# Kernel optimization log

Measured on AMD Instinct MI355X. Metric: run time of the kernel, lower is better.

## Reference

```python
import jax, jax.numpy as jnp
import numpy as np

B, S, W, H = 16, 512, 8, 768  # batch, seq_len, max_span width, hidden_dim


def setup_inputs() -> dict:
    key = jax.random.key(0)
    ks = jax.random.split(key, 6)
    return {
        "hidden": jax.random.normal(ks[0], (B, S, H), jnp.float32),
        "term_weight": jax.random.normal(ks[1], (H,), jnp.float32),
        "w1": jax.random.normal(ks[2], (H, 64), jnp.float32) * 0.02,
        "b1": jnp.zeros((64,), jnp.float32),
        "w2": jax.random.normal(ks[3], (64, 1), jnp.float32) * 0.05,
        "b2": jnp.zeros((1,), jnp.float32),
        "w_score": jax.random.normal(ks[4], (H, 2), jnp.float32) * 0.02,
        "b_score": jnp.zeros((2,), jnp.float32),
    }


def reference(hidden, term_weight, w1, b1, w2, b2, w_score, b_score):
    # TermAttention token logits: MLP(hidden * termWeight) depends only on the
    # token, not the span, so compute once per token instead of per span.
    ah = hidden * term_weight                                  # [B,S,H]
    tok_logit = (jax.nn.relu(ah @ w1 + b1) @ w2 + b2)[..., 0]  # [B,S]

    starts = jnp.arange(S)
    offs = jnp.arange(W)
    # candidate span (start s, width w) covers tokens s .. min(s+w, S-1)
    tok_idx = jnp.minimum(starts[:, None] + offs[None, :], S - 1)      # [S,W]
    span_len = jnp.minimum(offs[None, :] + 1, S - starts[:, None])    # [S,W]

    Lg = tok_logit[:, tok_idx]   # [B,S,W] gathered per-position logits
    Hg = hidden[:, tok_idx]      # [B,S,W,H] gathered per-position hiddens

    # pos_mask[s,w,j] = position j is inside span (s, width w)
    pos_mask = offs[None, None, :] < span_len[:, :, None]              # [S,W,W]
    logits = jnp.where(pos_mask[None], Lg[:, :, None, :], -jnp.inf)   # [B,S,W,W]
    attn = jax.nn.softmax(logits, axis=-1)                             # [B,S,W,W]

    # span embedding = attention-weighted sum of span token hiddens
    emb = jnp.einsum('bswj,bsjh->bswh', attn, Hg)                      # [B,S,W,H]
    scores = emb @ w_score + b_score                                   # [B,S,W,2]
    return scores
```

## Files before the change

kernel.cpp:

```cpp
#include <hip/hip_runtime.h>

#define S_LEN 512
#define H_DIM 768
#define BS_TOK 8192
#define NCOLS 80
#define KSPLIT 4
#define KSEG 192
#define KPAD 200
#define PSTRIDE 72
#define BM 32
#define TOKB 32

typedef __attribute__((ext_vector_type(8))) short short8v;
typedef __attribute__((ext_vector_type(4))) short short4v;
typedef __attribute__((ext_vector_type(4))) float f32x4;
typedef __attribute__((ext_vector_type(4))) _Float16 h4;

__device__ __forceinline__ short f2bf(float f) {
  union { float f; unsigned u; } x; x.f = f;
  unsigned r = x.u + 0x7fffu + ((x.u >> 16) & 1u);
  return (short)(r >> 16);
}

__global__ __launch_bounds__(128) void k1f(const float* __restrict__ hidden,
                                           const float* __restrict__ tw,
                                           const float* __restrict__ w1,
                                           const float* __restrict__ wsc,
                                           _Float16* __restrict__ part) {
  __shared__ short bs[NCOLS * KPAD];
  const int tid  = threadIdx.x;
  const int bid  = blockIdx.x;
  const int tile = bid >> 2;
  const int kseg = bid & 3;
  const int k0   = kseg * KSEG;

#pragma unroll
  for (int i = 0; i < 24; ++i) {
    int e = tid + 128 * i;
    int koff = e >> 4, c4 = e & 15;
    int k = k0 + koff;
    float twk = tw[k];
    float4 w = *reinterpret_cast<const float4*>(w1 + (size_t)k * 64 + c4 * 4);
    bs[(c4 * 4 + 0) * KPAD + koff] = f2bf(w.x * twk);
    bs[(c4 * 4 + 1) * KPAD + koff] = f2bf(w.y * twk);
    bs[(c4 * 4 + 2) * KPAD + koff] = f2bf(w.z * twk);
    bs[(c4 * 4 + 3) * KPAD + koff] = f2bf(w.w * twk);
  }
#pragma unroll
  for (int i = 0; i < 3; ++i) {
    int e = tid + 128 * i;
    if (e < 2 * KSEG) {
      int koff = e >> 1, c = e & 1;
      bs[(64 + c) * KPAD + koff] = f2bf(wsc[(size_t)(k0 + koff) * 2 + c]);
    }
  }
  for (int i = tid; i < 14 * KSEG; i += 128) {
    int c = 66 + i / KSEG, koff = i - (c - 66) * KSEG;
    bs[c * KPAD + koff] = 0;
  }
  __syncthreads();

  const int w    = tid >> 6;
  const int lane = tid & 63;
  const int ci   = lane & 15;
  const int g    = lane >> 4;
  const int kg   = g * 8;
  const int r0   = tile * BM + w * 16;

  f32x4 acc[5];
#pragma unroll
  for (int nt = 0; nt < 5; ++nt) acc[nt] = (f32x4){0.f, 0.f, 0.f, 0.f};

  const float* aptr = hidden + (size_t)(r0 + ci) * H_DIM + k0 + kg;
#pragma unroll
  for (int ks = 0; ks < KSEG; ks += 32) {
    float4 a0 = *reinterpret_cast<const float4*>(aptr + ks);
    float4 a1 = *reinterpret_cast<const float4*>(aptr + ks + 4);
    short8v av;
    av[0] = f2bf(a0.x); av[1] = f2bf(a0.y); av[2] = f2bf(a0.z); av[3] = f2bf(a0.w);
    av[4] = f2bf(a1.x); av[5] = f2bf(a1.y); av[6] = f2bf(a1.z); av[7] = f2bf(a1.w);
#pragma unroll
    for (int nt = 0; nt < 5; ++nt) {
      short8v bb = *reinterpret_cast<const short8v*>(&bs[(nt * 16 + ci) * KPAD + ks + kg]);
      acc[nt] = __builtin_amdgcn_mfma_f32_16x16x32_bf16(av, bb, acc[nt], 0, 0, 0);
    }
  }

  _Float16* pr = part + ((size_t)kseg * BS_TOK + r0) * PSTRIDE;
#pragma unroll
  for (int j = 0; j < 4; ++j) {
    int r = 4 * g + j;
#pragma unroll
    for (int nt = 0; nt < 4; ++nt)
      pr[r * PSTRIDE + nt * 16 + ci] = (_Float16)acc[nt][j];
    if (ci < 2) pr[r * PSTRIDE + 64 + ci] = (_Float16)acc[4][j];
  }
}

__global__ __launch_bounds__(256) void kB(const _Float16* __restrict__ part,
                                          const float* __restrict__ b1,
                                          const float* __restrict__ w2,
                                          const float* __restrict__ b2,
                                          const float* __restrict__ bsc,
                                          float* __restrict__ out) {
  __shared__ float lp[TOKB + 8][4];
  const int tid  = threadIdx.x;
  const int t0   = blockIdx.x * TOKB;
  const int w    = tid >> 6;
  const int lane = tid & 63;
  const int ci   = lane & 15;
  const int grp  = lane >> 4;
  const int base = w * 4 + grp;

#pragma unroll
  for (int pass = 0; pass < 3; ++pass) {
    int slot = pass * 16 + base;
    if (slot < TOKB + 7) {
      int tt = min(t0 + slot, BS_TOK - 1);
      f32x4 s = (f32x4){0.f, 0.f, 0.f, 0.f};
#pragma unroll
      for (int seg = 0; seg < KSPLIT; ++seg) {
        h4 v = *reinterpret_cast<const h4*>(
            part + ((size_t)seg * BS_TOK + tt) * PSTRIDE + 4 * ci);
        s[0] += (float)v[0]; s[1] += (float)v[1];
        s[2] += (float)v[2]; s[3] += (float)v[3];
      }
      const float4 bb = *reinterpret_cast<const float4*>(b1 + 4 * ci);
      const float4 ww = *reinterpret_cast<const float4*>(w2 + 4 * ci);
      float r = fmaxf(s[0] + bb.x, 0.f) * ww.x + fmaxf(s[1] + bb.y, 0.f) * ww.y +
                fmaxf(s[2] + bb.z, 0.f) * ww.z + fmaxf(s[3] + bb.w, 0.f) * ww.w;
#pragma unroll
      for (int msk = 1; msk < 16; msk <<= 1) r += __shfl_xor(r, msk, 64);
      if (ci == 0) lp[slot][0] = r + b2[0];
      if (ci < 2) {
        float pv = 0.f;
#pragma unroll
        for (int seg = 0; seg < KSPLIT; ++seg)
          pv += (float)part[((size_t)seg * BS_TOK + tt) * PSTRIDE + 64 + ci];
        lp[slot][1 + ci] = pv;
      }
    }
  }
  __syncthreads();

  if (tid < TOKB) {
    int t = t0 + tid;
    int s_ = t & (S_LEN - 1);
    int nmax = min(8, S_LEN - s_);
    float bs0 = bsc[0], bs1 = bsc[1];
    float m = lp[tid][0];
    float d = 1.f;
    float n0 = lp[tid][1], n1 = lp[tid][2];
    float o[16];
    o[0] = n0 + bs0; o[1] = n1 + bs1;
#pragma unroll
    for (int j = 1; j < 8; ++j) {
      if (j < nmax) {
        float L  = lp[tid + j][0];
        float nm = fmaxf(m, L);
        float sc = __expf(m - nm);
        float e  = __expf(L - nm);
        d  = d  * sc + e;
        n0 = n0 * sc + e * lp[tid + j][1];
        n1 = n1 * sc + e * lp[tid + j][2];
        m = nm;
      }
      float inv = 1.f / d;
      o[2 * j]     = n0 * inv + bs0;
      o[2 * j + 1] = n1 * inv + bs1;
    }
    float4* op = reinterpret_cast<float4*>(out + (size_t)t * 16);
#pragma unroll
    for (int i = 0; i < 4; ++i) op[i] = *reinterpret_cast<float4*>(&o[4 * i]);
  }
}


__global__ __launch_bounds__(256) void kprep(const float* __restrict__ tw,
                                             const float* __restrict__ w1,
                                             const float* __restrict__ wsc,
                                             short* __restrict__ wcat) {
  int i = blockIdx.x * 256 + threadIdx.x;
  if (i >= NCOLS * H_DIM) return;
  int c = i / H_DIM, k = i - c * H_DIM;
  float v = 0.f;
  if (c < 64)       v = tw[k] * w1[k * 64 + c];
  else if (c == 64) v = wsc[k * 2 + 0];
  else if (c == 65) v = wsc[k * 2 + 1];
  wcat[i] = f2bf(v);
}

__global__ __launch_bounds__(256) void k1s(const float* __restrict__ hidden,
                                           const short* __restrict__ wcat,
                                           const float* __restrict__ b1,
                                           const float* __restrict__ w2,
                                           const float* __restrict__ b2,
                                           float* __restrict__ logit,
                                           float* __restrict__ pbuf) {
  __shared__ short as[64 * 72];
  __shared__ short bss[NCOLS * 72];
  const int tid  = threadIdx.x;
  const int t0   = blockIdx.x * 64;
  const int w    = tid >> 6;
  const int lane = tid & 63;
  const int ci   = lane & 15;
  const int kg   = (lane >> 4) * 8;
  const int arow = w * 16 + ci;

  f32x4 acc[5];
#pragma unroll
  for (int nt = 0; nt < 5; ++nt) acc[nt] = (f32x4){0.f, 0.f, 0.f, 0.f};

  for (int cc = 0; cc < H_DIM / 64; ++cc) {
    const int k0 = cc * 64;
    __syncthreads();
#pragma unroll
    for (int i = 0; i < 4; ++i) {
      int f = tid + 256 * i;
      int r = f >> 4, c4 = f & 15;
      const float4 v = *reinterpret_cast<const float4*>(
          hidden + (size_t)(t0 + r) * H_DIM + k0 + c4 * 4);
      short4v bv;
      bv[0] = f2bf(v.x); bv[1] = f2bf(v.y); bv[2] = f2bf(v.z); bv[3] = f2bf(v.w);
      *reinterpret_cast<short4v*>(&as[r * 72 + c4 * 4]) = bv;
    }
    for (int i = tid; i < NCOLS * 8; i += 256) {
      int r = i >> 3, c8 = i & 7;
      short8v v = *reinterpret_cast<const short8v*>(wcat + r * H_DIM + k0 + c8 * 8);
      *reinterpret_cast<short8v*>(&bss[r * 72 + c8 * 8]) = v;
    }
    __syncthreads();
#pragma unroll
    for (int ks = 0; ks < 64; ks += 32) {
      short8v a = *reinterpret_cast<const short8v*>(&as[arow * 72 + ks + kg]);
#pragma unroll
      for (int nt = 0; nt < 5; ++nt) {
        short8v bb = *reinterpret_cast<const short8v*>(&bss[(nt * 16 + ci) * 72 + ks + kg]);
        acc[nt] = __builtin_amdgcn_mfma_f32_16x16x32_bf16(a, bb, acc[nt], 0, 0, 0);
      }
    }
  }

  const int g = lane >> 4;
  float lg[4];
#pragma unroll
  for (int j = 0; j < 4; ++j) {
    float sacc = 0.f;
#pragma unroll
    for (int nt = 0; nt < 4; ++nt) {
      int c = nt * 16 + ci;
      float z = acc[nt][j] + b1[c];
      z = fmaxf(z, 0.f);
      sacc += z * w2[c];
    }
#pragma unroll
    for (int msk = 1; msk < 16; msk <<= 1) sacc += __shfl_xor(sacc, msk, 64);
    lg[j] = sacc;
  }
  const float b2v = b2[0];
#pragma unroll
  for (int j = 0; j < 4; ++j) {
    int rg = t0 + w * 16 + 4 * g + j;
    if (ci == 0) {
      logit[rg] = lg[j] + b2v;
      pbuf[rg * 2 + 0] = acc[4][j];
    } else if (ci == 1) {
      pbuf[rg * 2 + 1] = acc[4][j];
    }
  }
}

__global__ __launch_bounds__(256) void k3g(const float* __restrict__ logit,
                                           const float* __restrict__ pbuf,
                                           const float* __restrict__ bsc,
                                           float* __restrict__ out) {
  int t = blockIdx.x * 256 + threadIdx.x;
  int s = t & (S_LEN - 1);
  int nmax = min(8, S_LEN - s);
  float bs0 = bsc[0], bs1 = bsc[1];
  float m = logit[t];
  float d = 1.f;
  float n0 = pbuf[2 * t], n1 = pbuf[2 * t + 1];
  float o[16];
  o[0] = n0 + bs0; o[1] = n1 + bs1;
#pragma unroll
  for (int j = 1; j < 8; ++j) {
    if (j < nmax) {
      float L  = logit[t + j];
      float nm = fmaxf(m, L);
      float sc = __expf(m - nm);
      float e  = __expf(L - nm);
      d  = d  * sc + e;
      n0 = n0 * sc + e * pbuf[2 * (t + j)];
      n1 = n1 * sc + e * pbuf[2 * (t + j) + 1];
      m = nm;
    }
    float inv = 1.f / d;
    o[2 * j]     = n0 * inv + bs0;
    o[2 * j + 1] = n1 * inv + bs1;
  }
  float4* op = reinterpret_cast<float4*>(out + (size_t)t * 16);
#pragma unroll
  for (int i = 0; i < 4; ++i) op[i] = *reinterpret_cast<float4*>(&o[4 * i]);
}


extern "C" void kernel_launch(void* const* d_in, const int* in_sizes, int n_in,
                              void* d_out, int out_size, void* d_ws, size_t ws_size,
                              hipStream_t stream) {
  const float* hidden = (const float*)d_in[0];
  const float* tw     = (const float*)d_in[1];
  const float* w1     = (const float*)d_in[2];
  const float* b1     = (const float*)d_in[3];
  const float* w2     = (const float*)d_in[4];
  const float* b2     = (const float*)d_in[5];
  const float* wsc    = (const float*)d_in[6];
  const float* bsc    = (const float*)d_in[7];
  float* out = (float*)d_out;
  char* ws = (char*)d_ws;

  const size_t part_bytes = (size_t)KSPLIT * BS_TOK * PSTRIDE * 2;

  if (ws_size >= part_bytes) {
    _Float16* part = (_Float16*)ws;
    k1f<<<(BS_TOK / BM) * KSPLIT, 128, 0, stream>>>(hidden, tw, w1, wsc, part);
    kB <<<BS_TOK / TOKB, 256, 0, stream>>>(part, b1, w2, b2, bsc, out);
  } else {
    short* wcat  = (short*)ws;
    float* logit = (float*)(ws + 131072);
    float* pbuf  = (float*)(ws + 131072 + 32768);
    kprep<<<(NCOLS * H_DIM + 255) / 256, 256, 0, stream>>>(tw, w1, wsc, wcat);
    k1s<<<BS_TOK / 64, 256, 0, stream>>>(hidden, wcat, b1, w2, b2, logit, pbuf);
    k3g<<<BS_TOK / 256, 256, 0, stream>>>(logit, pbuf, bsc, out);
  }
}
```

Baseline: 22.97 us.

## Precompute bf16 weight segments in a prep kernel and double k1f row tile

Moves the per-block scaling and bf16 conversion of term_weight*w1 and w_score out of k1f into a separate prep kernel that writes padded per-K-segment weight images to workspace. k1f now copies its segment into shared memory with vectorized 16-byte loads, and its row tile grows from 32 to 64 rows with 256 threads. This removes repeated conversion work across many blocks and halves the block count. In exchange it adds a kernel launch, needs more workspace, and lowers the number of blocks available to fill the GPU.

```diff
diff --git a/kernel.cpp b/kernel.cpp
--- a/kernel.cpp
+++ b/kernel.cpp
@@ -7,8 +7,9 @@
 #define KSPLIT 4
 #define KSEG 192
 #define KPAD 200
+#define WSEG (NCOLS * KPAD)
 #define PSTRIDE 72
-#define BM 32
+#define BM 64
 #define TOKB 32
 
 typedef __attribute__((ext_vector_type(8))) short short8v;
@@ -22,41 +23,46 @@
   return (short)(r >> 16);
 }
 
-__global__ __launch_bounds__(128) void k1f(const float* __restrict__ hidden,
-                                           const float* __restrict__ tw,
-                                           const float* __restrict__ w1,
-                                           const float* __restrict__ wsc,
+__global__ __launch_bounds__(256) void kprep(const float* __restrict__ tw,
+                                             const float* __restrict__ w1,
+                                             const float* __restrict__ wsc,
+                                             short* __restrict__ wcat) {
+  int i = blockIdx.x * 256 + threadIdx.x;
+  if (i >= KSPLIT * WSEG) return;
+  int kseg = i / WSEG;
+  int rem  = i - kseg * WSEG;
+  int c    = rem / KPAD;
+  int koff = rem - c * KPAD;
+  float v = 0.f;
+  if (koff < KSEG && c < 66) {
+    int k = kseg * KSEG + koff;
+    if (c < 64) v = tw[k] * w1[(size_t)k * 64 + c];
+    else        v = wsc[(size_t)k * 2 + (c - 64)];
+  }
+  wcat[i] = f2bf(v);
+}
+
+__global__ __launch_bounds__(256) void k1f(const float* __restrict__ hidden,
+                                           const short* __restrict__ wcat,
                                            _Float16* __restrict__ part) {
-  __shared__ short bs[NCOLS * KPAD];
+  __shared__ short bs[WSEG];
   const int tid  = threadIdx.x;
   const int bid  = blockIdx.x;
   const int tile = bid >> 2;
   const int kseg = bid & 3;
   const int k0   = kseg * KSEG;
 
-#pragma unroll
-  for (int i = 0; i < 24; ++i) {
-    int e = tid + 128 * i;
-    int koff = e >> 4, c4 = e & 15;
-    int k = k0 + koff;
-    float twk = tw[k];
-    float4 w = *reinterpret_cast<const float4*>(w1 + (size_t)k * 64 + c4 * 4);
-    bs[(c4 * 4 + 0) * KPAD + koff] = f2bf(w.x * twk);
-    bs[(c4 * 4 + 1) * KPAD + koff] = f2bf(w.y * twk);
-    bs[(c4 * 4 + 2) * KPAD + koff] = f2bf(w.z * twk);
-    bs[(c4 * 4 + 3) * KPAD + koff] = f2bf(w.w * twk);
-  }
-#pragma unroll
-  for (int i = 0; i < 3; ++i) {
-    int e = tid + 128 * i;
-    if (e < 2 * KSEG) {
-      int koff = e >> 1, c = e & 1;
-      bs[(64 + c) * KPAD + koff] = f2bf(wsc[(size_t)(k0 + koff) * 2 + c]);
-    }
-  }
-  for (int i = tid; i < 14 * KSEG; i += 128) {
-    int c = 66 + i / KSEG, koff = i - (c - 66) * KSEG;
-    bs[c * KPAD + koff] = 0;
+  const short* wseg = wcat + (size_t)kseg * WSEG;
+#pragma unroll
+  for (int i = 0; i < 7; ++i) {
+    int e = tid + 256 * i;
+    *reinterpret_cast<short8v*>(&bs[e * 8]) =
+        *reinterpret_cast<const short8v*>(wseg + (size_t)e * 8);
+  }
+  if (tid < 208) {
+    int e = 1792 + tid;
+    *reinterpret_cast<short8v*>(&bs[e * 8]) =
+        *reinterpret_cast<const short8v*>(wseg + (size_t)e * 8);
   }
   __syncthreads();
 
@@ -176,10 +182,10 @@
 }
 
 
-__global__ __launch_bounds__(256) void kprep(const float* __restrict__ tw,
-                                             const float* __restrict__ w1,
-                                             const float* __restrict__ wsc,
-                                             short* __restrict__ wcat) {
+__global__ __launch_bounds__(256) void kprepS(const float* __restrict__ tw,
+                                              const float* __restrict__ w1,
+                                              const float* __restrict__ wsc,
+                                              short* __restrict__ wcat) {
   int i = blockIdx.x * 256 + threadIdx.x;
   if (i >= NCOLS * H_DIM) return;
   int c = i / H_DIM, k = i - c * H_DIM;
@@ -320,16 +326,20 @@
   char* ws = (char*)d_ws;
 
   const size_t part_bytes = (size_t)KSPLIT * BS_TOK * PSTRIDE * 2;
-
-  if (ws_size >= part_bytes) {
+  const size_t wcat_bytes = (size_t)KSPLIT * WSEG * 2;
+  const size_t need_fast  = part_bytes + wcat_bytes;
+
+  if (ws_size >= need_fast) {
     _Float16* part = (_Float16*)ws;
-    k1f<<<(BS_TOK / BM) * KSPLIT, 128, 0, stream>>>(hidden, tw, w1, wsc, part);
-    kB <<<BS_TOK / TOKB, 256, 0, stream>>>(part, b1, w2, b2, bsc, out);
+    short* wcat    = (short*)(ws + part_bytes);
+    kprep<<<(KSPLIT * WSEG + 255) / 256, 256, 0, stream>>>(tw, w1, wsc, wcat);
+    k1f  <<<(BS_TOK / BM) * KSPLIT, 256, 0, stream>>>(hidden, wcat, part);
+    kB   <<<BS_TOK / TOKB, 256, 0, stream>>>(part, b1, w2, b2, bsc, out);
   } else {
     short* wcat  = (short*)ws;
     float* logit = (float*)(ws + 131072);
     float* pbuf  = (float*)(ws + 131072 + 32768);
-    kprep<<<(NCOLS * H_DIM + 255) / 256, 256, 0, stream>>>(tw, w1, wsc, wcat);
+    kprepS<<<(NCOLS * H_DIM + 255) / 256, 256, 0, stream>>>(tw, w1, wsc, wcat);
     k1s<<<BS_TOK / 64, 256, 0, stream>>>(hidden, wcat, b1, w2, b2, logit, pbuf);
     k3g<<<BS_TOK / 256, 256, 0, stream>>>(logit, pbuf, bsc, out);
   }
```

Measured after the change: 22.57 us. Within noise of the previous version (-1.7%).
